# Kernel optimization log

Measured on AMD Instinct MI355X. Metric: run time of the kernel, lower is better.

The kernel has to match this reference:

```python
import jax, jax.numpy as jnp
import numpy as np

SIMOTA_Q = 10
W_CLS, W_GEOM, W_IOU, W_DIST, W_THETA = 4.0, 5.0, 2.0, 1.0, 2.0
INVALID = -100000.0
LINE_HALF_WIDTH = 15.0


def _pairwise_line_iou(pred_xs, gt_xs):
    # pred_xs [B,N,S], gt_xs [B,M,S] -> iou [B,N,M] (CLRNet-style line IoU)
    p = pred_xs[:, :, None, :]  # [B,N,1,S]
    t = gt_xs[:, None, :, :]    # [B,1,M,S]
    inv = (p == INVALID) | (t == INVALID)
    ovr = jnp.minimum(p + LINE_HALF_WIDTH, t + LINE_HALF_WIDTH) - jnp.maximum(p - LINE_HALF_WIDTH, t - LINE_HALF_WIDTH)
    union = jnp.maximum(p + LINE_HALF_WIDTH, t + LINE_HALF_WIDTH) - jnp.minimum(p - LINE_HALF_WIDTH, t - LINE_HALF_WIDTH)
    ovr = jnp.where(inv, 0.0, ovr)
    union = jnp.where(inv, 0.0, union)
    return ovr.sum(-1) / (union.sum(-1) + 1e-9)


def setup_inputs() -> dict:
    key = jax.random.key(0)
    ks = jax.random.split(key, 12)
    B, N, M, S = 16, 1000, 24, 72
    img_w, img_h = 800, 320
    # preds: [logit0, logit1, start_y, start_x, theta(deg), length, delta_x*S]
    p = jnp.concatenate([
        jax.random.normal(ks[0], (B, N, 2)),
        jax.random.uniform(ks[1], (B, N, 1), minval=img_h * 0.4, maxval=img_h - 1.0),
        jax.random.uniform(ks[2], (B, N, 1), minval=0.0, maxval=img_w - 1.0),
        jax.random.uniform(ks[3], (B, N, 1), minval=20.0, maxval=160.0),
        jax.random.uniform(ks[4], (B, N, 1), minval=10.0, maxval=float(img_h)),
        jax.random.normal(ks[5], (B, N, S)) * 5.0,
    ], axis=-1)
    t = jnp.concatenate([
        jnp.zeros((B, M, 2)),
        jax.random.uniform(ks[6], (B, M, 1), minval=img_h * 0.5, maxval=img_h - 1.0),
        jax.random.uniform(ks[7], (B, M, 1), minval=50.0, maxval=img_w - 50.0),
        jax.random.uniform(ks[8], (B, M, 1), minval=30.0, maxval=150.0),
        jax.random.uniform(ks[9], (B, M, 1), minval=10.0, maxval=float(img_h)),
        jax.random.normal(ks[10], (B, M, S)) * 5.0,
    ], axis=-1)
    masks = jax.random.bernoulli(ks[11], 0.5, (B, M))
    return {"preds": p.astype(jnp.float32), "targets": t.astype(jnp.float32),
            "masks": masks, "img_w": img_w, "img_h": img_h}


def reference(preds, targets, masks, img_w, img_h):
    B, N, C = preds.shape
    M = targets.shape[1]
    S = C - 6
    dt = preds.dtype
    sample_ys = jnp.linspace(img_h - 1.0, 0.0, S, dtype=dt).reshape(1, 1, S)

    p_sy, p_sx, p_th, p_len = preds[..., 2], preds[..., 3], preds[..., 4], preds[..., 5]
    p_dx = preds[..., 6:]
    g_sy, g_sx, g_th = targets[..., 2], targets[..., 3], targets[..., 4]
    g_dx = targets[..., 6:]

    # absolute sample-x for preds and gts along row anchors
    p_tan = jnp.clip(jnp.tan(jnp.deg2rad(p_th)), -1000.0, 1000.0)
    p_xs = p_sx[..., None] + (p_sy[..., None] - sample_ys) * p_tan[..., None] + p_dx  # [B,N,S]
    g_tan = jnp.clip(jnp.tan(jnp.deg2rad(g_th)), -1000.0, 1000.0)
    g_xs = g_sx[..., None] + (g_sy[..., None] - sample_ys) * g_tan[..., None] + g_dx  # [B,M,S]

    p_valid = (sample_ys >= (p_sy - p_len)[..., None]) & (sample_ys <= p_sy[..., None])
    p_xs = jnp.where(p_valid, p_xs, INVALID)
    g_inv = (g_dx < -10000.0) | (g_xs < 0) | (g_xs >= img_w)
    g_xs = jnp.where(g_inv, INVALID, g_xs)

    ious = jnp.nan_to_num(_pairwise_line_iou(p_xs, g_xs), nan=0.0)  # [B,N,M]
    ious = jnp.where(masks[:, None, :], ious, 0.0)
    iou_cost = 1.0 - ious

    dx = (p_sx[:, :, None] - g_sx[:, None, :]) / (img_w - 1)
    dy = (p_sy[:, :, None] - g_sy[:, None, :]) / (img_h - 1)
    dist_cost = jnp.sqrt(dx * dx + dy * dy + 1e-8)
    theta_cost = jnp.abs((p_th[:, :, None] - g_th[:, None, :]) / 90.0)
    geom_cost = W_DIST * dist_cost + W_THETA * theta_cost

    score = jax.nn.softmax(preds[..., :2], axis=-1)[..., 1]
    cls_cost = -jnp.log(jnp.clip(score, 1e-8))[:, :, None]

    total = W_CLS * cls_cost + W_GEOM * geom_cost + W_IOU * iou_cost
    total = jnp.where(masks[:, None, :], total, 100000.0)

    # dynamic-k: since dynamic_ks <= SIMOTA_Q always, use fixed K (extra slots masked by k_mask)
    K = min(SIMOTA_Q, N)
    topk_ious, _ = jax.lax.top_k(jnp.swapaxes(ious, 1, 2), K)       # [B,M,K]
    dynamic_ks = jnp.clip(topk_ious.sum(-1).astype(jnp.int32), 1, N)  # [B,M]
    _, topk_idx = jax.lax.top_k(-jnp.swapaxes(total, 1, 2), K)      # smallest costs, [B,M,K]
    topk_idx = jnp.swapaxes(topk_idx, 1, 2)                         # [B,K,M]
    k_mask = jnp.arange(K)[None, :, None] < dynamic_ks[:, None, :]  # [B,K,M]

    b_ix = jnp.arange(B)[:, None, None]
    m_ix = jnp.arange(M)[None, None, :]
    matching = jnp.zeros((B, N, M), dt).at[b_ix, topk_idx, m_ix].set(k_mask.astype(dt))
    matching = jnp.where(masks[:, None, :], matching, 0.0)

    # conflict resolution: anchors matched to >1 gt keep only min-cost gt
    conflict = matching.sum(-1) > 1.0
    cost_inf = jnp.where(matching == 0.0, jnp.inf, total)
    min_idx = jnp.argmin(cost_inf, axis=2)
    matching = jnp.where(conflict[..., None], jax.nn.one_hot(min_idx, M, dtype=dt), matching)

    assigned = matching.sum(-1) > 0
    matched = jnp.argmax(matching, axis=2)
    matched = jnp.where(assigned, matched, -1)
    return assigned, matched
```

## Files before the change

kernel.cpp:

```cpp
#include <hip/hip_runtime.h>
#include <math.h>
#include <float.h>

#define Bb 16
#define Nn 1000
#define NP 1024
#define Mm 24
#define Ss 72
#define Cc 78
#define Kk 10
#define NCH 4
#define INVALIDF (-100000.0f)
#define DEG2RAD 0.017453292519943295f

struct Hdr { int mask_mode; int pad0; int pad1; int pad2; };

#define CHSZ       (Bb*Mm*NCH*Kk*4)
#define OFF_CHTOT  16
#define OFF_CHIDX  (OFF_CHTOT + CHSZ)
#define OFF_CHIOU  (OFF_CHIDX + CHSZ)
#define OFF_MOK    (OFF_CHIOU + CHSZ)
#define OFF_PMETA  ((OFF_MOK + Bb*Mm*4 + 255) & ~255)
#define OFF_PXS    (OFF_PMETA + Bb*NP*16)
#define WS6_NEEDED (OFF_PXS + Bb*Ss*NP*4)

__device__ __forceinline__ float read_dim(const void* p) {
    int v = *(const int*)p;
    if (v <= 0 || v > 1000000) v = (int)(*(const float*)p);
    return (float)v;
}

__device__ __forceinline__ bool mask_at(const void* m, int mode, int idx) {
    if (mode == 0) return ((const unsigned char*)m)[idx] != 0;
    if (mode == 1) return ((const int*)m)[idx] != 0;
    return ((const float*)m)[idx] != 0.0f;
}

__device__ __forceinline__ void bitonic64(float& v, int& i, const int lane) {
#pragma unroll
    for (int k = 2; k <= 64; k <<= 1) {
#pragma unroll
        for (int j = k >> 1; j >= 1; j >>= 1) {
            const float pv = __shfl_xor(v, j, 64);
            const int   pi = __shfl_xor(i, j, 64);
            const bool keepMin = (((lane & k) == 0) == ((lane & j) == 0));
            const bool meLess  = (v < pv) || (v == pv && i < pi);
            if (keepMin ? !meLess : meLess) { v = pv; i = pi; }
        }
    }
}

__device__ __forceinline__ void bitonic64v(float& v, const int lane) {
#pragma unroll
    for (int k = 2; k <= 64; k <<= 1) {
#pragma unroll
        for (int j = k >> 1; j >= 1; j >>= 1) {
            const float pv = __shfl_xor(v, j, 64);
            const bool keepMin = (((lane & k) == 0) == ((lane & j) == 0));
            if (keepMin ? (pv < v) : (pv > v)) v = pv;
        }
    }
}

__global__ __launch_bounds__(256) void k_prep2(
    const float* __restrict__ preds, const unsigned char* __restrict__ mb,
    const void* __restrict__ hp,
    Hdr* __restrict__ hdr, int* __restrict__ mok,
    float* __restrict__ pxs, float4* __restrict__ pmeta)
{
    __shared__ float lds[32 * Cc];
    __shared__ float ys[Ss];
    __shared__ float ssx[32], ssy[32], sptan[32], slo[32];
    __shared__ int s_nz, s_f32;

    const int tid = threadIdx.x;
    const int q = blockIdx.x;
    const int L = ((q & 7) << 6) | (q >> 3);
    const int b   = L >> 5;
    const int blk = L & 31;
    const int base_n = blk * 32;
    const int valid = (base_n + 32 <= Nn) ? 32 : (Nn - base_n);

    const float4* src4 = (const float4*)(preds + ((size_t)b * Nn + base_n) * Cc);
    float4* lds4 = (float4*)lds;
    const int n4 = (valid * Cc) / 4;
    for (int i = tid; i < n4; i += 256) lds4[i] = src4[i];

    const float ih = read_dim(hp);
    if (tid < Ss)
        ys[tid] = (float)((double)(ih - 1.0f) * (double)(Ss - 1 - tid) / (double)(Ss - 1));

    if (q == 0) {
        if (tid == 0) { s_nz = 0; s_f32 = 0; }
        __syncthreads();
        if (tid < (Bb * Mm) / 4) {
            const uchar4 c4 = *(const uchar4*)(mb + tid * 4);
            int nz = (c4.y ? 1 : 0) + (c4.z ? 1 : 0) + (c4.w ? 1 : 0);
            bool f = (c4.x == 0x80 || c4.x == 0x3f) || (c4.y == 0x80 || c4.y == 0x3f) ||
                     (c4.z == 0x80 || c4.z == 0x3f) || (c4.w == 0x80 || c4.w == 0x3f);
            if (nz) atomicAdd(&s_nz, nz);
            if (f)  atomicOr(&s_f32, 1);
        }
        __syncthreads();
        const int mode = (s_nz == 0) ? 1 : (s_f32 ? 2 : 0);
        if (tid == 0) hdr->mask_mode = mode;
        for (int i = tid; i < Bb * Mm; i += 256)
            mok[i] = mask_at(mb, mode, i) ? 1 : 0;
    }
    __syncthreads();

    if (tid < valid) {
        const float* pr = lds + tid * Cc;
        const float p0 = pr[0], p1 = pr[1];
        const float sy = pr[2], sx = pr[3], th = pr[4], len = pr[5];
        const float mx = fmaxf(p0, p1);
        const float e0 = expf(p0 - mx), e1 = expf(p1 - mx);
        float score = fmaxf(e1 / (e0 + e1), 1e-8f);
        const float cls = -logf(score);
        ssx[tid] = sx; ssy[tid] = sy;
        sptan[tid] = fminf(fmaxf(tanf(th * DEG2RAD), -1000.0f), 1000.0f);
        slo[tid] = sy - len;
        pmeta[(b << 10) | (base_n + tid)] = make_float4(cls, sx, sy, th);
    }
    __syncthreads();

    const int nn = tid & 31, srow = tid >> 5;
    if (nn < valid) {
        const int n = base_n + nn;
        const float sx = ssx[nn], sy = ssy[nn], ptan = sptan[nn], lo = slo[nn];
        const float* dxr = lds + nn * Cc + 6;
        for (int s = srow; s < Ss; s += 8) {
            const float y = ys[s];
            const float px = sx + (sy - y) * ptan + dxr[s];
            const bool valid_s = (y >= lo) && (y <= sy);
            pxs[(((size_t)b * Ss + s) << 10) | n] = valid_s ? px : INVALIDF;
        }
    }
}

__global__ __launch_bounds__(256) void k_colE4(
    const float* __restrict__ targs, const int* __restrict__ mok,
    const float* __restrict__ pxs, const float4* __restrict__ pmeta,
    const void* __restrict__ wp, const void* __restrict__ hp,
    float* __restrict__ chtot, int* __restrict__ chidx, float* __restrict__ chiou)
{
    __shared__ float gx[Ss];
    __shared__ float wtot[4][Kk];
    __shared__ int   widx[4][Kk];
    __shared__ float wiou[4][Kk];

    const int P = blockIdx.x;
    const int L = (P & 7) * 192 + (P >> 3);
    const int col   = L >> 2;
    const int chunk = L & 3;
    const int b     = col / Mm;
    const int tid   = threadIdx.x;

    if (!mok[col]) return;

    const float iw = read_dim(wp);
    const float ih = read_dim(hp);
    const float* tg = targs + (size_t)col * Cc;
    const float g_sy = tg[2], g_sx = tg[3], g_th = tg[4];
    const float g_tan = fminf(fmaxf(tanf(g_th * DEG2RAD), -1000.0f), 1000.0f);

    if (tid < Ss) {
        const float y = (float)((double)(ih - 1.0f) * (double)(Ss - 1 - tid) / (double)(Ss - 1));
        const float gdx = tg[6 + tid];
        float v = g_sx + (g_sy - y) * g_tan + gdx;
        if (gdx < -10000.0f || v < 0.0f || v >= iw) v = INVALIDF;
        gx[tid] = v;
    }
    __syncthreads();

    const int n = chunk * 256 + tid;
    float ov = 0.0f, un = 0.0f;
    const float* pxb = pxs + (((size_t)b * Ss) << 10);
#pragma unroll
    for (int bat = 0; bat < 3; ++bat) {
        float pxr[24];
#pragma unroll
        for (int u = 0; u < 24; ++u)
            pxr[u] = pxb[((bat * 24 + u) << 10) | n];
#pragma unroll
        for (int u = 0; u < 24; ++u) {
            const float g = gx[bat * 24 + u];
            const float px = pxr[u];
            if (g != INVALIDF && px != INVALIDF) {
                const float d = fabsf(px - g);
                ov += 30.0f - d;
                un += 30.0f + d;
            }
        }
    }

    const float4 me = pmeta[(b << 10) + n];
    const float iouv = ov / (un + 1e-9f);
    const float dxn = (me.y - g_sx) / (iw - 1.0f);
    const float dyn = (me.z - g_sy) / (ih - 1.0f);
    const float dist = sqrtf(dxn * dxn + dyn * dyn + 1e-8f);
    const float theta = fabsf((me.w - g_th) / 90.0f);
    const float geom = 1.0f * dist + 2.0f * theta;
    const float t = 4.0f * me.x + 5.0f * geom + 2.0f * (1.0f - iouv);

    const int w = tid >> 6, lane = tid & 63;

    float v1 = (n < Nn) ? t : FLT_MAX;     int i1 = n;
    bitonic64(v1, i1, lane);
    if (lane < Kk) { wtot[w][lane] = v1; widx[w][lane] = i1; }

    float v2 = (n < Nn) ? -iouv : FLT_MAX;
    bitonic64v(v2, lane);
    if (lane < Kk) wiou[w][lane] = v2;
    __syncthreads();

    const int obase = L * Kk;
    if (w == 0) {
        float v = FLT_MAX; int i = 0x7fffffff;
        if (lane < NCH * Kk) { v = wtot[lane / Kk][lane % Kk]; i = widx[lane / Kk][lane % Kk]; }
        bitonic64(v, i, lane);
        if (lane < Kk) { chtot[obase + lane] = v; chidx[obase + lane] = i; }
    } else if (w == 1) {
        float v = FLT_MAX;
        if (lane < NCH * Kk) v = wiou[lane / Kk][lane % Kk];
        bitonic64v(v, lane);
        if (lane < Kk) chiou[obase + lane] = -v;
    }
}

__global__ __launch_bounds__(1024) void k_final2(
    const int* __restrict__ mok,
    const float* __restrict__ chtot, const int* __restrict__ chidx,
    const float* __restrict__ chiou, int* __restrict__ out)
{
    __shared__ float stot[Mm * NCH * Kk];
    __shared__ int   sidx[Mm * NCH * Kk];
    __shared__ float siou[Mm * NCH * Kk];
    __shared__ int   s_sel[Mm * Kk];
    __shared__ float s_tot[Mm * Kk];
    __shared__ int   s_dk[Mm];
    __shared__ int   maskok[Mm];

    const int b   = blockIdx.x;
    const int tid = threadIdx.x;

    const int bbase = b * (Mm * NCH * Kk);
    if (tid < Mm * NCH * Kk) {
        stot[tid] = chtot[bbase + tid];
        sidx[tid] = chidx[bbase + tid];
        siou[tid] = chiou[bbase + tid];
    }
    if (tid < Mm) maskok[tid] = mok[b * Mm + tid];
    __syncthreads();

    const int w = tid >> 6, lane = tid & 63;
    for (int m = w; m < Mm; m += 16) {
        if (!maskok[m]) {
            if (lane == 0) s_dk[m] = 0;
            continue;
        }
        float v = FLT_MAX; int i = 0x7fffffff;
        if (lane < NCH * Kk) { v = stot[m * NCH * Kk + lane]; i = sidx[m * NCH * Kk + lane]; }
        bitonic64(v, i, lane);
        if (lane < Kk) { s_sel[m * Kk + lane] = i; s_tot[m * Kk + lane] = v; }

        float v2 = FLT_MAX;
        if (lane < NCH * Kk) v2 = -siou[m * NCH * Kk + lane];
        bitonic64v(v2, lane);
        float isum = 0.0f;
#pragma unroll
        for (int k = 0; k < Kk; ++k) isum += -__shfl(v2, k, 64);
        if (lane == 0) {
            int dk = (int)isum;
            dk = (dk < 1) ? 1 : (dk > Kk ? Kk : dk);
            s_dk[m] = dk;
        }
    }
    __syncthreads();

    if (tid < Nn) {
        const int n = tid;
        int cnt = 0, firstm = -1, bestm = -1;
        float bestv = FLT_MAX;
        for (int m = 0; m < Mm; ++m) {
            const int dk = s_dk[m];
            for (int k = 0; k < dk; ++k) {
                if (s_sel[m * Kk + k] == n) {
                    const float tv = s_tot[m * Kk + k];
                    cnt++;
                    if (firstm < 0) firstm = m;
                    if (tv < bestv) { bestv = tv; bestm = m; }
                    break;
                }
            }
        }
        int matched;
        if (cnt == 0)      matched = -1;
        else if (cnt == 1) matched = firstm;
        else               matched = bestm;

        const int gid = b * Nn + n;
        out[gid]           = (cnt > 0) ? 1 : 0;
        out[Bb * Nn + gid] = matched;
    }
}

#define OFF_FSELK   16
#define OFF_FSELTOT (OFF_FSELK + Bb*Mm*Kk*4)
#define OFF_FDYNK   (OFF_FSELTOT + Bb*Mm*Kk*4)

__global__ void k_detect_fb(const unsigned char* __restrict__ mb, Hdr* __restrict__ hdr) {
    int nz_off = 0; bool f32pat = false;
    for (int i = 0; i < Bb * Mm; ++i) {
        unsigned char c = mb[i];
        if ((i & 3) && c) nz_off++;
        if (c == 0x80 || c == 0x3f) f32pat = true;
    }
    hdr->mask_mode = (nz_off == 0) ? 1 : (f32pat ? 2 : 0);
}

__global__ __launch_bounds__(256) void k_col_fb(
    const float* __restrict__ preds, const float* __restrict__ targs,
    const void* __restrict__ masks, const Hdr* __restrict__ hdr,
    const void* __restrict__ wp, const void* __restrict__ hp,
    int* __restrict__ selk, float* __restrict__ seltot, int* __restrict__ dynk)
{
    __shared__ float ys[Ss];
    __shared__ float gx[Ss];
    __shared__ float iou_s[Nn];
    __shared__ float tot_s[Nn];
    __shared__ float rv[256];
    __shared__ int   ri[256];

    const int bm = blockIdx.x;
    const int b  = bm / Mm;
    const int tid = threadIdx.x;
    const float iw = read_dim(wp);
    const float ih = read_dim(hp);

    if (!mask_at(masks, hdr->mask_mode, bm)) {
        if (tid == 0) dynk[bm] = 0;
        return;
    }
    if (tid < Ss)
        ys[tid] = (float)((double)(ih - 1.0f) * (double)(Ss - 1 - tid) / (double)(Ss - 1));
    __syncthreads();

    const float* tg = targs + (size_t)bm * Cc;
    const float g_sy = tg[2], g_sx = tg[3], g_th = tg[4];
    const float g_tan = fminf(fmaxf(tanf(g_th * DEG2RAD), -1000.0f), 1000.0f);
    if (tid < Ss) {
        float gdx = tg[6 + tid];
        float v = g_sx + (g_sy - ys[tid]) * g_tan + gdx;
        if (gdx < -10000.0f || v < 0.0f || v >= iw) v = INVALIDF;
        gx[tid] = v;
    }
    __syncthreads();

    for (int n = tid; n < Nn; n += 256) {
        const float* pr = preds + ((size_t)b * Nn + n) * Cc;
        const float p0 = pr[0], p1 = pr[1];
        const float sy = pr[2], sx = pr[3], th = pr[4], len = pr[5];
        const float mx = fmaxf(p0, p1);
        const float e0 = expf(p0 - mx), e1 = expf(p1 - mx);
        float score = fmaxf(e1 / (e0 + e1), 1e-8f);
        const float cls = -logf(score);
        const float ptan = fminf(fmaxf(tanf(th * DEG2RAD), -1000.0f), 1000.0f);
        const float lo = sy - len;
        float ov = 0.0f, un = 0.0f;
        for (int s = 0; s < Ss; ++s) {
            const float y = ys[s];
            const float t = gx[s];
            if (y >= lo && y <= sy && t != INVALIDF) {
                const float px = sx + (sy - y) * ptan + pr[6 + s];
                if (px != INVALIDF) {
                    const float d = fabsf(px - t);
                    ov += 30.0f - d;
                    un += 30.0f + d;
                }
            }
        }
        const float iou = ov / (un + 1e-9f);
        const float dxn = (sx - g_sx) / (iw - 1.0f);
        const float dyn = (sy - g_sy) / (ih - 1.0f);
        const float dist = sqrtf(dxn * dxn + dyn * dyn + 1e-8f);
        const float theta = fabsf((th - g_th) / 90.0f);
        const float tot = 4.0f * cls + 5.0f * (1.0f * dist + 2.0f * theta) + 2.0f * (1.0f - iou);
        iou_s[n] = iou;
        tot_s[n] = tot;
    }
    __syncthreads();

    for (int k = 0; k < Kk; ++k) {
        float bv = FLT_MAX; int bi = 0x7fffffff;
        for (int n = tid; n < Nn; n += 256) {
            const float v = tot_s[n];
            if (v < bv) { bv = v; bi = n; }
        }
        rv[tid] = bv; ri[tid] = bi;
        __syncthreads();
        for (int off = 128; off > 0; off >>= 1) {
            if (tid < off) {
                const float v2 = rv[tid + off]; const int i2 = ri[tid + off];
                if (v2 < rv[tid] || (v2 == rv[tid] && i2 < ri[tid])) { rv[tid] = v2; ri[tid] = i2; }
            }
            __syncthreads();
        }
        if (tid == 0) {
            const int c = ri[0];
            selk[bm * Kk + k] = c;
            seltot[bm * Kk + k] = tot_s[c];
            tot_s[c] = FLT_MAX;
        }
        __syncthreads();
    }

    float isum = 0.0f;
    for (int k = 0; k < Kk; ++k) {
        float bv = -FLT_MAX; int bi = 0x7fffffff;
        for (int n = tid; n < Nn; n += 256) {
            const float v = iou_s[n];
            if (v > bv) { bv = v; bi = n; }
        }
        rv[tid] = bv; ri[tid] = bi;
        __syncthreads();
        for (int off = 128; off > 0; off >>= 1) {
            if (tid < off) {
                const float v2 = rv[tid + off]; const int i2 = ri[tid + off];
                if (v2 > rv[tid] || (v2 == rv[tid] && i2 < ri[tid])) { rv[tid] = v2; ri[tid] = i2; }
            }
            __syncthreads();
        }
        if (tid == 0) {
            const int c = ri[0];
            isum += iou_s[c];
            iou_s[c] = -FLT_MAX;
        }
        __syncthreads();
    }
    if (tid == 0) {
        int dk = (int)isum;
        dk = (dk < 1) ? 1 : (dk > Nn ? Nn : dk);
        dynk[bm] = dk;
    }
}

__global__ __launch_bounds__(256) void k_resolve_fb(
    const int* __restrict__ selk, const float* __restrict__ seltot,
    const int* __restrict__ dynk, int* __restrict__ out)
{
    const int gid = blockIdx.x * 256 + threadIdx.x;
    if (gid >= Bb * Nn) return;
    const int b = gid / Nn;
    const int n = gid % Nn;

    int cnt = 0, firstm = -1, bestm = -1;
    float bestv = FLT_MAX;
    for (int m = 0; m < Mm; ++m) {
        const int bm = b * Mm + m;
        const int dk = dynk[bm];
        for (int k = 0; k < dk && k < Kk; ++k) {
            if (selk[bm * Kk + k] == n) {
                const float tv = seltot[bm * Kk + k];
                cnt++;
                if (firstm < 0) firstm = m;
                if (tv < bestv) { bestv = tv; bestm = m; }
                break;
            }
        }
    }
    int matched;
    if (cnt == 0)      matched = -1;
    else if (cnt == 1) matched = firstm;
    else               matched = bestm;

    out[gid]           = (cnt > 0) ? 1 : 0;
    out[Bb * Nn + gid] = matched;
}

extern "C" void kernel_launch(void* const* d_in, const int* in_sizes, int n_in,
                              void* d_out, int out_size, void* d_ws, size_t ws_size,
                              hipStream_t stream) {
    const float* preds = (const float*)d_in[0];
    const float* targs = (const float*)d_in[1];
    const void*  masks = d_in[2];
    const void*  wp    = d_in[3];
    const void*  hp    = d_in[4];
    int* out = (int*)d_out;

    char* ws = (char*)d_ws;
    Hdr* hdr = (Hdr*)ws;

    if (ws_size >= (size_t)WS6_NEEDED) {
        float*  chtot = (float*)(ws + OFF_CHTOT);
        int*    chidx = (int*)(ws + OFF_CHIDX);
        float*  chiou = (float*)(ws + OFF_CHIOU);
        int*    mok   = (int*)(ws + OFF_MOK);
        float4* pmeta = (float4*)(ws + OFF_PMETA);
        float*  pxs   = (float*)(ws + OFF_PXS);

        k_prep2<<<512, 256, 0, stream>>>(preds, (const unsigned char*)masks, hp,
                                         hdr, mok, pxs, pmeta);
        k_colE4<<<Bb * Mm * NCH, 256, 0, stream>>>(targs, mok, pxs, pmeta,
                                                   wp, hp, chtot, chidx, chiou);
        k_final2<<<Bb, 1024, 0, stream>>>(mok, chtot, chidx, chiou, out);
    } else {
        int*   selk   = (int*)(ws + OFF_FSELK);
        float* seltot = (float*)(ws + OFF_FSELTOT);
        int*   dynk   = (int*)(ws + OFF_FDYNK);
        k_detect_fb<<<1, 1, 0, stream>>>((const unsigned char*)masks, hdr);
        k_col_fb<<<Bb * Mm, 256, 0, stream>>>(preds, targs, masks, hdr, wp, hp,
                                              selk, seltot, dynk);
        k_resolve_fb<<<(Bb * Nn + 255) / 256, 256, 0, stream>>>(selk, seltot, dynk, out);
    }
}
```

Baseline: 44.37 us.

## Split column top-k into 128-thread blocks and add per-column merge kernel

The column kernel now runs 3072 blocks of 128 threads. Each wave writes its own 64-anchor top-10 straight to global memory, replacing the in-block cross-wave merge. A new per-column merge kernel (384 blocks) reduces the 16 partial lists to the final top-k and dynamic k, so the single-block-per-batch final kernel only resolves conflicts. This spreads the merge work over many blocks to cut the serial tail in the final kernel, at the cost of one extra launch and more intermediate global traffic.

```diff
diff --git a/kernel.cpp b/kernel.cpp
--- a/kernel.cpp
+++ b/kernel.cpp
@@ -9,20 +9,23 @@
 #define Ss 72
 #define Cc 78
 #define Kk 10
-#define NCH 4
+#define NL 16
 #define INVALIDF (-100000.0f)
 #define DEG2RAD 0.017453292519943295f
 
 struct Hdr { int mask_mode; int pad0; int pad1; int pad2; };
 
-#define CHSZ       (Bb*Mm*NCH*Kk*4)
+#define LSZ        (Bb*Mm*NL*Kk*4)
 #define OFF_CHTOT  16
-#define OFF_CHIDX  (OFF_CHTOT + CHSZ)
-#define OFF_CHIOU  (OFF_CHIDX + CHSZ)
-#define OFF_MOK    (OFF_CHIOU + CHSZ)
-#define OFF_PMETA  ((OFF_MOK + Bb*Mm*4 + 255) & ~255)
+#define OFF_CHIDX  (OFF_CHTOT + LSZ)
+#define OFF_CHIOU  (OFF_CHIDX + LSZ)
+#define OFF_MOK    (OFF_CHIOU + LSZ)
+#define OFF_MSEL   (OFF_MOK + Bb*Mm*4)
+#define OFF_MTOT   (OFF_MSEL + Bb*Mm*Kk*4)
+#define OFF_MDK    (OFF_MTOT + Bb*Mm*Kk*4)
+#define OFF_PMETA  ((OFF_MDK + Bb*Mm*4 + 255) & ~255)
 #define OFF_PXS    (OFF_PMETA + Bb*NP*16)
-#define WS6_NEEDED (OFF_PXS + Bb*Ss*NP*4)
+#define WS7_NEEDED (OFF_PXS + Bb*Ss*NP*4)
 
 __device__ __forceinline__ float read_dim(const void* p) {
     int v = *(const int*)p;
@@ -138,21 +141,18 @@
     }
 }
 
-__global__ __launch_bounds__(256) void k_colE4(
+__global__ __launch_bounds__(128) void k_colJ(
     const float* __restrict__ targs, const int* __restrict__ mok,
     const float* __restrict__ pxs, const float4* __restrict__ pmeta,
     const void* __restrict__ wp, const void* __restrict__ hp,
     float* __restrict__ chtot, int* __restrict__ chidx, float* __restrict__ chiou)
 {
     __shared__ float gx[Ss];
-    __shared__ float wtot[4][Kk];
-    __shared__ int   widx[4][Kk];
-    __shared__ float wiou[4][Kk];
 
     const int P = blockIdx.x;
-    const int L = (P & 7) * 192 + (P >> 3);
-    const int col   = L >> 2;
-    const int chunk = L & 3;
+    const int L = (P & 7) * 384 + (P >> 3);
+    const int col   = L >> 3;
+    const int cpair = L & 7;
     const int b     = col / Mm;
     const int tid   = threadIdx.x;
 
@@ -173,7 +173,10 @@
     }
     __syncthreads();
 
-    const int n = chunk * 256 + tid;
+    const int w = tid >> 6, lane = tid & 63;
+    const int chunk = cpair * 2 + w;
+    const int n = (chunk << 6) | lane;
+
     float ov = 0.0f, un = 0.0f;
     const float* pxb = pxs + (((size_t)b * Ss) << 10);
 #pragma unroll
@@ -203,79 +206,103 @@
     const float geom = 1.0f * dist + 2.0f * theta;
     const float t = 4.0f * me.x + 5.0f * geom + 2.0f * (1.0f - iouv);
 
-    const int w = tid >> 6, lane = tid & 63;
+    const int obase = col * (NL * Kk) + chunk * Kk;
 
     float v1 = (n < Nn) ? t : FLT_MAX;     int i1 = n;
     bitonic64(v1, i1, lane);
-    if (lane < Kk) { wtot[w][lane] = v1; widx[w][lane] = i1; }
+    if (lane < Kk) { chtot[obase + lane] = v1; chidx[obase + lane] = i1; }
 
     float v2 = (n < Nn) ? -iouv : FLT_MAX;
     bitonic64v(v2, lane);
-    if (lane < Kk) wiou[w][lane] = v2;
-    __syncthreads();
-
-    const int obase = L * Kk;
-    if (w == 0) {
-        float v = FLT_MAX; int i = 0x7fffffff;
-        if (lane < NCH * Kk) { v = wtot[lane / Kk][lane % Kk]; i = widx[lane / Kk][lane % Kk]; }
-        bitonic64(v, i, lane);
-        if (lane < Kk) { chtot[obase + lane] = v; chidx[obase + lane] = i; }
-    } else if (w == 1) {
-        float v = FLT_MAX;
-        if (lane < NCH * Kk) v = wiou[lane / Kk][lane % Kk];
-        bitonic64v(v, lane);
-        if (lane < Kk) chiou[obase + lane] = -v;
-    }
-}
-
-__global__ __launch_bounds__(1024) void k_final2(
+    if (lane < Kk) chiou[obase + lane] = v2;
+}
+
+__global__ __launch_bounds__(128) void k_merge(
     const int* __restrict__ mok,
     const float* __restrict__ chtot, const int* __restrict__ chidx,
-    const float* __restrict__ chiou, int* __restrict__ out)
+    const float* __restrict__ chiou,
+    int* __restrict__ msel, float* __restrict__ mtot, int* __restrict__ mdk)
 {
-    __shared__ float stot[Mm * NCH * Kk];
-    __shared__ int   sidx[Mm * NCH * Kk];
-    __shared__ float siou[Mm * NCH * Kk];
+    const int P = blockIdx.x;
+    const int col = (P & 7) * 48 + (P >> 3);
+    const int tid = threadIdx.x;
+    const int w = tid >> 6, lane = tid & 63;
+
+    if (!mok[col]) {
+        if (tid == 0) mdk[col] = 0;
+        return;
+    }
+    const int base = col * (NL * Kk);
+    const int g = lane / 10, o = lane - g * 10;
+
+    if (w == 0) {
+        float tA, tB, tC, tD; int iA, iB, iC, iD;
+        tA = (lane < 40) ? chtot[base + lane]       : FLT_MAX;
+        iA = (lane < 40) ? chidx[base + lane]       : 0x7fffffff;
+        bitonic64(tA, iA, lane);
+        tB = (lane < 40) ? chtot[base + 40 + lane]  : FLT_MAX;
+        iB = (lane < 40) ? chidx[base + 40 + lane]  : 0x7fffffff;
+        bitonic64(tB, iB, lane);
+        tC = (lane < 40) ? chtot[base + 80 + lane]  : FLT_MAX;
+        iC = (lane < 40) ? chidx[base + 80 + lane]  : 0x7fffffff;
+        bitonic64(tC, iC, lane);
+        tD = (lane < 40) ? chtot[base + 120 + lane] : FLT_MAX;
+        iD = (lane < 40) ? chidx[base + 120 + lane] : 0x7fffffff;
+        bitonic64(tD, iD, lane);
+
+        const float vA = __shfl(tA, o, 64), vB = __shfl(tB, o, 64);
+        const float vC = __shfl(tC, o, 64), vD = __shfl(tD, o, 64);
+        const int   jA = __shfl(iA, o, 64), jB = __shfl(iB, o, 64);
+        const int   jC = __shfl(iC, o, 64), jD = __shfl(iD, o, 64);
+        float v = FLT_MAX; int i = 0x7fffffff;
+        if      (g == 0) { v = vA; i = jA; }
+        else if (g == 1) { v = vB; i = jB; }
+        else if (g == 2) { v = vC; i = jC; }
+        else if (g == 3) { v = vD; i = jD; }
+        bitonic64(v, i, lane);
+        if (lane < Kk) { msel[col * Kk + lane] = i; mtot[col * Kk + lane] = v; }
+    } else {
+        float tA, tB, tC, tD;
+        tA = (lane < 40) ? chiou[base + lane]       : FLT_MAX;  bitonic64v(tA, lane);
+        tB = (lane < 40) ? chiou[base + 40 + lane]  : FLT_MAX;  bitonic64v(tB, lane);
+        tC = (lane < 40) ? chiou[base + 80 + lane]  : FLT_MAX;  bitonic64v(tC, lane);
+        tD = (lane < 40) ? chiou[base + 120 + lane] : FLT_MAX;  bitonic64v(tD, lane);
+
+        const float vA = __shfl(tA, o, 64), vB = __shfl(tB, o, 64);
+        const float vC = __shfl(tC, o, 64), vD = __shfl(tD, o, 64);
+        float v = FLT_MAX;
+        if      (g == 0) v = vA;
+        else if (g == 1) v = vB;
+        else if (g == 2) v = vC;
+        else if (g == 3) v = vD;
+        bitonic64v(v, lane);
+        float isum = 0.0f;
+#pragma unroll
+        for (int k = 0; k < Kk; ++k) isum += -__shfl(v, k, 64);
+        if (lane == 0) {
+            int dk = (int)isum;
+            dk = (dk < 1) ? 1 : (dk > Kk ? Kk : dk);
+            mdk[col] = dk;
+        }
+    }
+}
+
+__global__ __launch_bounds__(1024) void k_resolve4(
+    const int* __restrict__ msel, const float* __restrict__ mtot,
+    const int* __restrict__ mdk, int* __restrict__ out)
+{
     __shared__ int   s_sel[Mm * Kk];
     __shared__ float s_tot[Mm * Kk];
     __shared__ int   s_dk[Mm];
-    __shared__ int   maskok[Mm];
 
     const int b   = blockIdx.x;
     const int tid = threadIdx.x;
 
-    const int bbase = b * (Mm * NCH * Kk);
-    if (tid < Mm * NCH * Kk) {
-        stot[tid] = chtot[bbase + tid];
-        sidx[tid] = chidx[bbase + tid];
-        siou[tid] = chiou[bbase + tid];
-    }
-    if (tid < Mm) maskok[tid] = mok[b * Mm + tid];
-    __syncthreads();
-
-    const int w = tid >> 6, lane = tid & 63;
-    for (int m = w; m < Mm; m += 16) {
-        if (!maskok[m]) {
-            if (lane == 0) s_dk[m] = 0;
-            continue;
-        }
-        float v = FLT_MAX; int i = 0x7fffffff;
-        if (lane < NCH * Kk) { v = stot[m * NCH * Kk + lane]; i = sidx[m * NCH * Kk + lane]; }
-        bitonic64(v, i, lane);
-        if (lane < Kk) { s_sel[m * Kk + lane] = i; s_tot[m * Kk + lane] = v; }
-
-        float v2 = FLT_MAX;
-        if (lane < NCH * Kk) v2 = -siou[m * NCH * Kk + lane];
-        bitonic64v(v2, lane);
-        float isum = 0.0f;
-#pragma unroll
-        for (int k = 0; k < Kk; ++k) isum += -__shfl(v2, k, 64);
-        if (lane == 0) {
-            int dk = (int)isum;
-            dk = (dk < 1) ? 1 : (dk > Kk ? Kk : dk);
-            s_dk[m] = dk;
-        }
-    }
+    if (tid < Mm * Kk) {
+        s_sel[tid] = msel[b * Mm * Kk + tid];
+        s_tot[tid] = mtot[b * Mm * Kk + tid];
+    }
+    if (tid < Mm) s_dk[tid] = mdk[b * Mm + tid];
     __syncthreads();
 
     if (tid < Nn) {
@@ -491,19 +518,24 @@
     char* ws = (char*)d_ws;
     Hdr* hdr = (Hdr*)ws;
 
-    if (ws_size >= (size_t)WS6_NEEDED) {
+    if (ws_size >= (size_t)WS7_NEEDED) {
         float*  chtot = (float*)(ws + OFF_CHTOT);
         int*    chidx = (int*)(ws + OFF_CHIDX);
         float*  chiou = (float*)(ws + OFF_CHIOU);
         int*    mok   = (int*)(ws + OFF_MOK);
+        int*    msel  = (int*)(ws + OFF_MSEL);
+        float*  mtot  = (float*)(ws + OFF_MTOT);
+        int*    mdk   = (int*)(ws + OFF_MDK);
         float4* pmeta = (float4*)(ws + OFF_PMETA);
         float*  pxs   = (float*)(ws + OFF_PXS);
 
         k_prep2<<<512, 256, 0, stream>>>(preds, (const unsigned char*)masks, hp,
                                          hdr, mok, pxs, pmeta);
-        k_colE4<<<Bb * Mm * NCH, 256, 0, stream>>>(targs, mok, pxs, pmeta,
-                                                   wp, hp, chtot, chidx, chiou);
-        k_final2<<<Bb, 1024, 0, stream>>>(mok, chtot, chidx, chiou, out);
+        k_colJ<<<Bb * Mm * 8, 128, 0, stream>>>(targs, mok, pxs, pmeta,
+                                                wp, hp, chtot, chidx, chiou);
+        k_merge<<<Bb * Mm, 128, 0, stream>>>(mok, chtot, chidx, chiou,
+                                             msel, mtot, mdk);
+        k_resolve4<<<Bb, 1024, 0, stream>>>(msel, mtot, mdk, out);
     } else {
         int*   selk   = (int*)(ws + OFF_FSELK);
         float* seltot = (float*)(ws + OFF_FSELTOT);
```

New measurement: 46.36 us. +4.5%, slower.
